# Optimization experiments

Measured on AMD Instinct MI355X. Metric: run time of the kernel, lower is better.

Reference implementation:

```python
import jax, jax.numpy as jnp
import numpy as np

RADIUS = 0.5   # first SetConv radius in PC_encoder
NSAMPLE = 16   # neighbors per ball


def setup_inputs() -> dict:
    key = jax.random.key(0)
    k = jax.random.split(key, 6)
    B, N, M = 4, 16384, 4096
    xyz = jax.random.normal(k[0], (B, N, 3), dtype=jnp.float32)
    feat = jax.random.normal(k[1], (B, N, 3), dtype=jnp.float32)
    fps_idx = jax.random.randint(k[2], (B, M), 0, N)
    W1 = jax.random.normal(k[3], (6, 32), dtype=jnp.float32) * 0.1
    b1 = jnp.zeros((32,), dtype=jnp.float32)
    W2 = jax.random.normal(k[4], (32, 32), dtype=jnp.float32) * 0.1
    b2 = jnp.zeros((32,), dtype=jnp.float32)
    return {"xyz": xyz, "feat": feat, "fps_idx": fps_idx,
            "W1": W1, "b1": b1, "W2": W2, "b2": b2}


def _ball_query(new_xyz, xyz, radius, k):
    # new_xyz: [B,M,3], xyz: [B,N,3] -> neighbor indices [B,M,K]
    B, N, _ = xyz.shape
    d2 = (jnp.sum(new_xyz ** 2, -1)[:, :, None]
          + jnp.sum(xyz ** 2, -1)[:, None, :]
          - 2.0 * jnp.einsum('bmc,bnc->bmn', new_xyz, xyz))  # [B,M,N]
    # pointnet2 ball_query picks the first k points (by index) inside the ball
    scores = jnp.where(d2 <= radius * radius,
                       jnp.arange(N, dtype=jnp.float32)[None, None, :],
                       jnp.float32(N))
    neg_top, idx = jax.lax.top_k(-scores, k)      # k smallest index-scores
    valid = neg_top > -jnp.float32(N)
    first = idx[..., :1]                           # pad missing with first hit
    return jnp.where(valid, idx, first)            # [B,M,K] int32


def _gather_groups(x, grp_idx):
    # x: [B,N,C], grp_idx: [B,M,K] -> [B,M,K,C]
    B, M, K = grp_idx.shape
    flat = jnp.take_along_axis(x, grp_idx.reshape(B, M * K)[..., None], axis=1)
    return flat.reshape(B, M, K, x.shape[-1])


def reference(xyz, feat, fps_idx, W1, b1, W2, b2):
    # SetConv(radius=0.5, npoint=N/4, nsample=16, in_feat=3, mlp=[32,32])
    new_xyz = jnp.take_along_axis(xyz, fps_idx[..., None], axis=1)   # [B,M,3]
    grp_idx = _ball_query(new_xyz, xyz, RADIUS, NSAMPLE)              # [B,M,K]
    grouped_xyz = _gather_groups(xyz, grp_idx)                        # [B,M,K,3]
    grouped_feat = _gather_groups(feat, grp_idx)                      # [B,M,K,3]
    rel = grouped_xyz - new_xyz[:, :, None, :]                        # local coords
    h = jnp.concatenate([rel, grouped_feat], axis=-1)                 # [B,M,K,6]
    act = lambda x: jax.nn.leaky_relu(x, 0.1)
    h = act(h @ W1 + b1)                                              # [B,M,K,32]
    h = act(h @ W2 + b2)                                              # [B,M,K,32]
    new_feat = jnp.max(h, axis=2)                                     # [B,M,32]
    return new_feat
```

## Files before the change

### kernel.cpp

```cpp
#include <hip/hip_runtime.h>


constexpr int N_PTS = 16384;
constexpr int M_Q   = 4096;
constexpr int KNN   = 16;
constexpr int TOTAL_Q = 4 * M_Q;
constexpr int TOTAL_P = 4 * N_PTS;

constexpr size_t WS_PKX   = 0;
constexpr size_t WS_PKF   = WS_PKX + (size_t)TOTAL_P * 16;
constexpr size_t WS_LONG  = WS_PKF + (size_t)TOTAL_P * 16;
constexpr size_t WS_SHORT = WS_LONG + (size_t)TOTAL_Q * 4;
constexpr size_t WS_CNTS  = WS_SHORT + (size_t)TOTAL_Q * 4;
constexpr size_t WS_NEED  = WS_CNTS + 64;

__global__ __launch_bounds__(256) void prep_kernel(
    const float* __restrict__ xyz, const float* __restrict__ feat,
    const int* __restrict__ fps,
    float4* __restrict__ pkX, float4* __restrict__ pkF,
    int* __restrict__ longL, int* __restrict__ shortL, int* __restrict__ cnts)
{
    const int i = blockIdx.x * 256 + threadIdx.x;
    const int lane = threadIdx.x & 63;
    const unsigned long long lt_mask = (1ull << lane) - 1ull;

    if (i < TOTAL_P) {
        const float x = xyz[i * 3 + 0], y = xyz[i * 3 + 1], z = xyz[i * 3 + 2];
        const float sq = __fadd_rn(__fadd_rn(__fmul_rn(x, x), __fmul_rn(y, y)),
                                   __fmul_rn(z, z));
        pkX[i] = make_float4(x, y, z, sq);
        pkF[i] = make_float4(feat[i * 3 + 0], feat[i * 3 + 1], feat[i * 3 + 2], 0.0f);
    }

    if (i < TOTAL_Q) {
        const int q = i;
        const int b = q >> 12;
        const int pidx = fps[q];
        const size_t base3 = ((size_t)b * N_PTS + pidx) * 3;
        const float x = xyz[base3 + 0], y = xyz[base3 + 1], z = xyz[base3 + 2];
        const float sq = __fadd_rn(__fadd_rn(__fmul_rn(x, x), __fmul_rn(y, y)),
                                   __fmul_rn(z, z));
        const bool isLong = (sq > 5.5f);

        const unsigned long long mkL = __ballot(isLong);
        int baseL = 0;
        if (lane == 0 && mkL) baseL = atomicAdd(&cnts[0], (int)__popcll(mkL));
        baseL = __shfl(baseL, 0, 64);
        if (isLong) longL[baseL + __popcll(mkL & lt_mask)] = q;

        const unsigned long long mkS = ~mkL;
        int baseS = 0;
        if (lane == 0 && mkS) baseS = atomicAdd(&cnts[1], (int)__popcll(mkS));
        baseS = __shfl(baseS, 0, 64);
        if (!isLong) shortL[baseS + __popcll(mkS & lt_mask)] = q;
    }
}

#define LOAD8(R, P, P2)                                          \
    {                                                            \
        _Pragma("unroll")                                        \
        for (int j = 0; j < 4; ++j) R[j] = (P)[j * 64];          \
        _Pragma("unroll")                                        \
        for (int j = 0; j < 4; ++j) R[4 + j] = (P2)[j * 64];     \
    }

#define PROC8(R, CB)                                                          \
    {                                                                         \
        _Pragma("unroll")                                                     \
        for (int j = 0; j < 8; ++j) {                                         \
            float dot = __fmul_rn(qx, R[j].x);                                \
            dot = __builtin_fmaf(qy, R[j].y, dot);                            \
            dot = __builtin_fmaf(qz, R[j].z, dot);                            \
            const float d2 = __fsub_rn(__fadd_rn(sqq, R[j].w),                \
                                       __fmul_rn(2.0f, dot));                 \
            const bool hit = (d2 <= 0.25f);                                   \
            const unsigned long long mk = __ballot(hit);                      \
            if (hit) {                                                        \
                const int pos = count + __popcll(mk & lt_mask);               \
                if (pos < KNN) sNbr[wave][pos] = (CB) + j * 64 + lane;        \
            }                                                                 \
            count += (int)__popcll(mk);                                       \
        }                                                                     \
    }

__global__ __launch_bounds__(256) void pe_flow_main_kernel(
    const float4* __restrict__ pkX, const float4* __restrict__ pkF,
    const int*   __restrict__ fps,
    const int*   __restrict__ longL, const int* __restrict__ shortL,
    const int*   __restrict__ cnts,
    const float* __restrict__ W1, const float* __restrict__ b1,
    const float* __restrict__ W2, const float* __restrict__ b2,
    float* __restrict__ out)
{
    __shared__ float sW1[192];
    __shared__ float sW2[1024];
    __shared__ float sb1[32];
    __shared__ float sb2[32];
    __shared__ int   sNbr[4][KNN];

    const int tid = threadIdx.x;
    if (tid < 192) sW1[tid] = W1[tid];
    for (int i = tid; i < 1024; i += 256) sW2[i] = W2[i];
    if (tid < 32) { sb1[tid] = b1[tid]; sb2[tid] = b2[tid]; }
    __syncthreads();

    const int wave = tid >> 6;
    const int lane = tid & 63;
    const unsigned long long lt_mask = (1ull << lane) - 1ull;

    const int w = blockIdx.x * 4 + wave;
    const int nLong = cnts[0];
    const int q = (w < nLong) ? longL[w] : shortL[w - nLong];
    const int b = q >> 12;

    const float4* pX = pkX + (size_t)b * N_PTS;
    const float4* pF = pkF + (size_t)b * N_PTS;

    const int pidx = fps[q];
    const float4 Q = pX[pidx];
    const float qx = Q.x, qy = Q.y, qz = Q.z, sqq = Q.w;

    int count = 0;
    {
        const float4* pA  = pX + lane;
        const float4* pA2 = pA + 256;
        const float4* pB  = pA + 512;
        const float4* pB2 = pA + 768;
        float4 ra[8], rb[8];

        LOAD8(ra, pA, pA2);
        __builtin_amdgcn_sched_barrier(0);

        for (int base = 0; base < N_PTS; base += 1024) {
            LOAD8(rb, pB, pB2);
            __builtin_amdgcn_sched_barrier(0);
            PROC8(ra, base);
            if (count >= KNN) break;

            pA += 1024; pA2 += 1024;
            if (base + 1024 < N_PTS) {
                LOAD8(ra, pA, pA2);
                __builtin_amdgcn_sched_barrier(0);
            }
            PROC8(rb, base + 512);
            if (count >= KNN) break;
            pB += 1024; pB2 += 1024;
        }
    }
    if (count < KNN) {
        const int first = sNbr[wave][0];
        if (lane >= count && lane < KNN) sNbr[wave][lane] = first;
    }

    const int k = lane >> 2;
    const int co = (lane & 3) * 8;
    const int ni = sNbr[wave][k];

    const float4 gx = pX[ni];
    const float4 gf = pF[ni];
    const float in0 = gx.x - qx;
    const float in1 = gx.y - qy;
    const float in2 = gx.z - qz;

    float h1[8];
    #pragma unroll
    for (int i = 0; i < 8; ++i) {
        float a = sb1[co + i];
        a += in0  * sW1[0 * 32 + co + i];
        a += in1  * sW1[1 * 32 + co + i];
        a += in2  * sW1[2 * 32 + co + i];
        a += gf.x * sW1[3 * 32 + co + i];
        a += gf.y * sW1[4 * 32 + co + i];
        a += gf.z * sW1[5 * 32 + co + i];
        h1[i] = (a >= 0.0f) ? a : 0.1f * a;
    }

    float h2[8];
    #pragma unroll
    for (int i = 0; i < 8; ++i) h2[i] = sb2[co + i];
    const int baseLane = lane & ~3;
    #pragma unroll
    for (int jj = 0; jj < 8; ++jj) {
        #pragma unroll
        for (int g = 0; g < 4; ++g) {
            const float v = __shfl(h1[jj], baseLane + g, 64);
            const int row = g * 8 + jj;
            #pragma unroll
            for (int i = 0; i < 8; ++i)
                h2[i] += v * sW2[row * 32 + co + i];
        }
    }

    #pragma unroll
    for (int i = 0; i < 8; ++i) {
        float v = h2[i];
        v = (v >= 0.0f) ? v : 0.1f * v;
        v = fmaxf(v, __shfl_xor(v, 4, 64));
        v = fmaxf(v, __shfl_xor(v, 8, 64));
        v = fmaxf(v, __shfl_xor(v, 16, 64));
        v = fmaxf(v, __shfl_xor(v, 32, 64));
        h2[i] = v;
    }

    if (k == 0) {
        float* op = out + (size_t)q * 32 + co;
        #pragma unroll
        for (int i = 0; i < 8; ++i) op[i] = h2[i];
    }
}

__global__ __launch_bounds__(256) void pe_flow_fused_kernel(
    const float* __restrict__ xyz, const float* __restrict__ feat,
    const int* __restrict__ fps,
    const float* __restrict__ W1, const float* __restrict__ b1,
    const float* __restrict__ W2, const float* __restrict__ b2,
    float* __restrict__ out)
{
    __shared__ float sW1[192];
    __shared__ float sW2[1024];
    __shared__ float sb1[32];
    __shared__ float sb2[32];
    __shared__ int   sNbr[4][KNN];

    const int tid = threadIdx.x;
    if (tid < 192) sW1[tid] = W1[tid];
    for (int i = tid; i < 1024; i += 256) sW2[i] = W2[i];
    if (tid < 32) { sb1[tid] = b1[tid]; sb2[tid] = b2[tid]; }
    __syncthreads();

    const int wave = tid >> 6;
    const int lane = tid & 63;
    const int q = blockIdx.x * 4 + wave;
    const int b = q >> 12;
    const int m = q & (M_Q - 1);

    const float* xb = xyz  + (size_t)b * N_PTS * 3;
    const float* fb = feat + (size_t)b * N_PTS * 3;

    const int pidx = fps[b * M_Q + m];
    const float qx = xb[pidx * 3 + 0];
    const float qy = xb[pidx * 3 + 1];
    const float qz = xb[pidx * 3 + 2];
    const float sq_q = __fadd_rn(__fadd_rn(__fmul_rn(qx, qx), __fmul_rn(qy, qy)),
                                 __fmul_rn(qz, qz));

    int count = 0;
    const unsigned long long lt_mask = (1ull << lane) - 1ull;
    for (int base = 0; base < N_PTS; base += 64) {
        const int i = base + lane;
        const float px = xb[i * 3 + 0];
        const float py = xb[i * 3 + 1];
        const float pz = xb[i * 3 + 2];
        const float sq_p = __fadd_rn(__fadd_rn(__fmul_rn(px, px), __fmul_rn(py, py)),
                                     __fmul_rn(pz, pz));
        float dot = __fmul_rn(qx, px);
        dot = __builtin_fmaf(qy, py, dot);
        dot = __builtin_fmaf(qz, pz, dot);
        const float d2 = __fsub_rn(__fadd_rn(sq_q, sq_p), __fmul_rn(2.0f, dot));
        const bool hit = (d2 <= 0.25f);
        const unsigned long long mk = __ballot(hit);
        if (hit) {
            const int pos = count + __popcll(mk & lt_mask);
            if (pos < KNN) sNbr[wave][pos] = i;
        }
        count += (int)__popcll(mk);
        if (count >= KNN) break;
    }
    if (count < KNN) {
        const int first = sNbr[wave][0];
        if (lane >= count && lane < KNN) sNbr[wave][lane] = first;
    }

    const int k = lane >> 2;
    const int co = (lane & 3) * 8;
    const int ni = sNbr[wave][k];

    const float in0 = xb[ni * 3 + 0] - qx;
    const float in1 = xb[ni * 3 + 1] - qy;
    const float in2 = xb[ni * 3 + 2] - qz;
    const float in3 = fb[ni * 3 + 0];
    const float in4 = fb[ni * 3 + 1];
    const float in5 = fb[ni * 3 + 2];

    float h1[8];
    #pragma unroll
    for (int i = 0; i < 8; ++i) {
        float a = sb1[co + i];
        a += in0 * sW1[0 * 32 + co + i];
        a += in1 * sW1[1 * 32 + co + i];
        a += in2 * sW1[2 * 32 + co + i];
        a += in3 * sW1[3 * 32 + co + i];
        a += in4 * sW1[4 * 32 + co + i];
        a += in5 * sW1[5 * 32 + co + i];
        h1[i] = (a >= 0.0f) ? a : 0.1f * a;
    }

    float h2[8];
    #pragma unroll
    for (int i = 0; i < 8; ++i) h2[i] = sb2[co + i];
    const int baseLane = lane & ~3;
    #pragma unroll
    for (int jj = 0; jj < 8; ++jj) {
        #pragma unroll
        for (int g = 0; g < 4; ++g) {
            const float v = __shfl(h1[jj], baseLane + g, 64);
            const int row = g * 8 + jj;
            #pragma unroll
            for (int i = 0; i < 8; ++i)
                h2[i] += v * sW2[row * 32 + co + i];
        }
    }

    #pragma unroll
    for (int i = 0; i < 8; ++i) {
        float v = h2[i];
        v = (v >= 0.0f) ? v : 0.1f * v;
        v = fmaxf(v, __shfl_xor(v, 4, 64));
        v = fmaxf(v, __shfl_xor(v, 8, 64));
        v = fmaxf(v, __shfl_xor(v, 16, 64));
        v = fmaxf(v, __shfl_xor(v, 32, 64));
        h2[i] = v;
    }

    if (k == 0) {
        float* op = out + (size_t)q * 32 + co;
        #pragma unroll
        for (int i = 0; i < 8; ++i) op[i] = h2[i];
    }
}

extern "C" void kernel_launch(void* const* d_in, const int* in_sizes, int n_in,
                              void* d_out, int out_size, void* d_ws, size_t ws_size,
                              hipStream_t stream) {
    const float* xyz  = (const float*)d_in[0];
    const float* feat = (const float*)d_in[1];
    const int*   fps  = (const int*)d_in[2];
    const float* W1   = (const float*)d_in[3];
    const float* b1   = (const float*)d_in[4];
    const float* W2   = (const float*)d_in[5];
    const float* b2   = (const float*)d_in[6];
    float* out = (float*)d_out;

    if (ws_size < WS_NEED) {
        pe_flow_fused_kernel<<<TOTAL_Q / 4, 256, 0, stream>>>(
            xyz, feat, fps, W1, b1, W2, b2, out);
        return;
    }

    char* ws = (char*)d_ws;
    float4* pkX  = (float4*)(ws + WS_PKX);
    float4* pkF  = (float4*)(ws + WS_PKF);
    int* longL   = (int*)(ws + WS_LONG);
    int* shortL  = (int*)(ws + WS_SHORT);
    int* cnts    = (int*)(ws + WS_CNTS);

    hipMemsetAsync(cnts, 0, 8, stream);
    prep_kernel<<<TOTAL_P / 256, 256, 0, stream>>>(
        xyz, feat, fps, pkX, pkF, longL, shortL, cnts);
    pe_flow_main_kernel<<<TOTAL_Q / 4, 256, 0, stream>>>(
        pkX, pkF, fps, longL, shortL, cnts, W1, b1, W2, b2, out);
}
```

Measured before the change: 72.30 us.

## Bucket queries by radius into 8 bins; drop packed feat and LDS weight staging

Query scheduling moves from a two-way long/short split to eight buckets keyed on squared distance from the origin. Bucket 7 is dispatched first, so the expected longest ball-query scans start earliest and the load balances better. The prep kernel no longer packs features into float4, and the main kernel reads raw feat directly. MLP weights are now read from global memory with float4 loads instead of being staged into shared memory, which removes a __syncthreads and the LDS setup. The trade-off is repeated global or cache weight reads and a few extra atomics in prep.

```diff
diff --git a/kernel.cpp b/kernel.cpp
--- a/kernel.cpp
+++ b/kernel.cpp
@@ -6,19 +6,16 @@
 constexpr int KNN   = 16;
 constexpr int TOTAL_Q = 4 * M_Q;
 constexpr int TOTAL_P = 4 * N_PTS;
+constexpr int NBKT   = 8;
 
 constexpr size_t WS_PKX   = 0;
-constexpr size_t WS_PKF   = WS_PKX + (size_t)TOTAL_P * 16;
-constexpr size_t WS_LONG  = WS_PKF + (size_t)TOTAL_P * 16;
-constexpr size_t WS_SHORT = WS_LONG + (size_t)TOTAL_Q * 4;
-constexpr size_t WS_CNTS  = WS_SHORT + (size_t)TOTAL_Q * 4;
+constexpr size_t WS_LISTS = WS_PKX + (size_t)TOTAL_P * 16;
+constexpr size_t WS_CNTS  = WS_LISTS + (size_t)NBKT * TOTAL_Q * 4;
 constexpr size_t WS_NEED  = WS_CNTS + 64;
 
 __global__ __launch_bounds__(256) void prep_kernel(
-    const float* __restrict__ xyz, const float* __restrict__ feat,
-    const int* __restrict__ fps,
-    float4* __restrict__ pkX, float4* __restrict__ pkF,
-    int* __restrict__ longL, int* __restrict__ shortL, int* __restrict__ cnts)
+    const float* __restrict__ xyz, const int* __restrict__ fps,
+    float4* __restrict__ pkX, int* __restrict__ lists, int* __restrict__ cnts)
 {
     const int i = blockIdx.x * 256 + threadIdx.x;
     const int lane = threadIdx.x & 63;
@@ -29,30 +26,29 @@
         const float sq = __fadd_rn(__fadd_rn(__fmul_rn(x, x), __fmul_rn(y, y)),
                                    __fmul_rn(z, z));
         pkX[i] = make_float4(x, y, z, sq);
-        pkF[i] = make_float4(feat[i * 3 + 0], feat[i * 3 + 1], feat[i * 3 + 2], 0.0f);
     }
 
     if (i < TOTAL_Q) {
-        const int q = i;
-        const int b = q >> 12;
-        const int pidx = fps[q];
+        const int b = i >> 12;
+        const int pidx = fps[i];
         const size_t base3 = ((size_t)b * N_PTS + pidx) * 3;
         const float x = xyz[base3 + 0], y = xyz[base3 + 1], z = xyz[base3 + 2];
-        const float sq = __fadd_rn(__fadd_rn(__fmul_rn(x, x), __fmul_rn(y, y)),
-                                   __fmul_rn(z, z));
-        const bool isLong = (sq > 5.5f);
-
-        const unsigned long long mkL = __ballot(isLong);
-        int baseL = 0;
-        if (lane == 0 && mkL) baseL = atomicAdd(&cnts[0], (int)__popcll(mkL));
-        baseL = __shfl(baseL, 0, 64);
-        if (isLong) longL[baseL + __popcll(mkL & lt_mask)] = q;
-
-        const unsigned long long mkS = ~mkL;
-        int baseS = 0;
-        if (lane == 0 && mkS) baseS = atomicAdd(&cnts[1], (int)__popcll(mkS));
-        baseS = __shfl(baseS, 0, 64);
-        if (!isLong) shortL[baseS + __popcll(mkS & lt_mask)] = q;
+        const float s = __fadd_rn(__fadd_rn(__fmul_rn(x, x), __fmul_rn(y, y)),
+                                  __fmul_rn(z, z));
+        int key = (int)s;
+        key = key < 0 ? 0 : (key > NBKT - 1 ? NBKT - 1 : key);
+
+        #pragma unroll
+        for (int bb = 0; bb < NBKT; ++bb) {
+            const bool mine = (key == bb);
+            const unsigned long long mk = __ballot(mine);
+            if (mk) {
+                int base = 0;
+                if (lane == 0) base = atomicAdd(&cnts[bb], (int)__popcll(mk));
+                base = __shfl(base, 0, 64);
+                if (mine) lists[bb * TOTAL_Q + base + __popcll(mk & lt_mask)] = i;
+            }
+        }
     }
 }
 
@@ -84,37 +80,32 @@
     }
 
 __global__ __launch_bounds__(256) void pe_flow_main_kernel(
-    const float4* __restrict__ pkX, const float4* __restrict__ pkF,
+    const float4* __restrict__ pkX, const float* __restrict__ feat,
     const int*   __restrict__ fps,
-    const int*   __restrict__ longL, const int* __restrict__ shortL,
-    const int*   __restrict__ cnts,
+    const int*   __restrict__ lists, const int* __restrict__ cnts,
     const float* __restrict__ W1, const float* __restrict__ b1,
     const float* __restrict__ W2, const float* __restrict__ b2,
     float* __restrict__ out)
 {
-    __shared__ float sW1[192];
-    __shared__ float sW2[1024];
-    __shared__ float sb1[32];
-    __shared__ float sb2[32];
-    __shared__ int   sNbr[4][KNN];
-
-    const int tid = threadIdx.x;
-    if (tid < 192) sW1[tid] = W1[tid];
-    for (int i = tid; i < 1024; i += 256) sW2[i] = W2[i];
-    if (tid < 32) { sb1[tid] = b1[tid]; sb2[tid] = b2[tid]; }
-    __syncthreads();
-
+    __shared__ int sNbr[4][KNN];
+
+    const int tid  = threadIdx.x;
     const int wave = tid >> 6;
     const int lane = tid & 63;
     const unsigned long long lt_mask = (1ull << lane) - 1ull;
 
     const int w = blockIdx.x * 4 + wave;
-    const int nLong = cnts[0];
-    const int q = (w < nLong) ? longL[w] : shortL[w - nLong];
+    int q = 0, off = 0;
+    #pragma unroll
+    for (int bb = NBKT - 1; bb >= 0; --bb) {
+        const int c = cnts[bb];
+        const int idx = w - off;
+        if (idx >= 0 && idx < c) q = lists[bb * TOTAL_Q + idx];
+        off += c;
+    }
     const int b = q >> 12;
 
     const float4* pX = pkX + (size_t)b * N_PTS;
-    const float4* pF = pkF + (size_t)b * N_PTS;
 
     const int pidx = fps[q];
     const float4 Q = pX[pidx];
@@ -152,32 +143,39 @@
         if (lane >= count && lane < KNN) sNbr[wave][lane] = first;
     }
 
-    const int k = lane >> 2;
+    const int k  = lane >> 2;
     const int co = (lane & 3) * 8;
     const int ni = sNbr[wave][k];
 
     const float4 gx = pX[ni];
-    const float4 gf = pF[ni];
+    const size_t f3 = ((size_t)b * N_PTS + ni) * 3;
     const float in0 = gx.x - qx;
     const float in1 = gx.y - qy;
     const float in2 = gx.z - qz;
-
+    const float in3 = feat[f3 + 0];
+    const float in4 = feat[f3 + 1];
+    const float in5 = feat[f3 + 2];
+    const float in[6] = {in0, in1, in2, in3, in4, in5};
+
+    float4 h1a = *(const float4*)(b1 + co);
+    float4 h1b = *(const float4*)(b1 + co + 4);
+    #pragma unroll
+    for (int r = 0; r < 6; ++r) {
+        const float4 wa = *(const float4*)(W1 + r * 32 + co);
+        const float4 wb = *(const float4*)(W1 + r * 32 + co + 4);
+        h1a.x += in[r] * wa.x; h1a.y += in[r] * wa.y;
+        h1a.z += in[r] * wa.z; h1a.w += in[r] * wa.w;
+        h1b.x += in[r] * wb.x; h1b.y += in[r] * wb.y;
+        h1b.z += in[r] * wb.z; h1b.w += in[r] * wb.w;
+    }
     float h1[8];
-    #pragma unroll
-    for (int i = 0; i < 8; ++i) {
-        float a = sb1[co + i];
-        a += in0  * sW1[0 * 32 + co + i];
-        a += in1  * sW1[1 * 32 + co + i];
-        a += in2  * sW1[2 * 32 + co + i];
-        a += gf.x * sW1[3 * 32 + co + i];
-        a += gf.y * sW1[4 * 32 + co + i];
-        a += gf.z * sW1[5 * 32 + co + i];
-        h1[i] = (a >= 0.0f) ? a : 0.1f * a;
-    }
-
-    float h2[8];
-    #pragma unroll
-    for (int i = 0; i < 8; ++i) h2[i] = sb2[co + i];
+    h1[0] = h1a.x; h1[1] = h1a.y; h1[2] = h1a.z; h1[3] = h1a.w;
+    h1[4] = h1b.x; h1[5] = h1b.y; h1[6] = h1b.z; h1[7] = h1b.w;
+    #pragma unroll
+    for (int i = 0; i < 8; ++i) h1[i] = (h1[i] >= 0.0f) ? h1[i] : 0.1f * h1[i];
+
+    float4 h2a = *(const float4*)(b2 + co);
+    float4 h2b = *(const float4*)(b2 + co + 4);
     const int baseLane = lane & ~3;
     #pragma unroll
     for (int jj = 0; jj < 8; ++jj) {
@@ -185,12 +183,18 @@
         for (int g = 0; g < 4; ++g) {
             const float v = __shfl(h1[jj], baseLane + g, 64);
             const int row = g * 8 + jj;
-            #pragma unroll
-            for (int i = 0; i < 8; ++i)
-                h2[i] += v * sW2[row * 32 + co + i];
-        }
-    }
-
+            const float4 wa = *(const float4*)(W2 + row * 32 + co);
+            const float4 wb = *(const float4*)(W2 + row * 32 + co + 4);
+            h2a.x += v * wa.x; h2a.y += v * wa.y;
+            h2a.z += v * wa.z; h2a.w += v * wa.w;
+            h2b.x += v * wb.x; h2b.y += v * wb.y;
+            h2b.z += v * wb.z; h2b.w += v * wb.w;
+        }
+    }
+
+    float h2[8];
+    h2[0] = h2a.x; h2[1] = h2a.y; h2[2] = h2a.z; h2[3] = h2a.w;
+    h2[4] = h2b.x; h2[5] = h2b.y; h2[6] = h2b.z; h2[7] = h2b.w;
     #pragma unroll
     for (int i = 0; i < 8; ++i) {
         float v = h2[i];
@@ -348,15 +352,12 @@
     }
 
     char* ws = (char*)d_ws;
-    float4* pkX  = (float4*)(ws + WS_PKX);
-    float4* pkF  = (float4*)(ws + WS_PKF);
-    int* longL   = (int*)(ws + WS_LONG);
-    int* shortL  = (int*)(ws + WS_SHORT);
-    int* cnts    = (int*)(ws + WS_CNTS);
-
-    hipMemsetAsync(cnts, 0, 8, stream);
-    prep_kernel<<<TOTAL_P / 256, 256, 0, stream>>>(
-        xyz, feat, fps, pkX, pkF, longL, shortL, cnts);
+    float4* pkX = (float4*)(ws + WS_PKX);
+    int* lists  = (int*)(ws + WS_LISTS);
+    int* cnts   = (int*)(ws + WS_CNTS);
+
+    hipMemsetAsync(cnts, 0, NBKT * 4, stream);
+    prep_kernel<<<TOTAL_P / 256, 256, 0, stream>>>(xyz, fps, pkX, lists, cnts);
     pe_flow_main_kernel<<<TOTAL_Q / 4, 256, 0, stream>>>(
-        pkX, pkF, fps, longL, shortL, cnts, W1, b1, W2, b2, out);
+        pkX, feat, fps, lists, cnts, W1, b1, W2, b2, out);
 }
```

Result: slower. 110.2 us (+52.4%).
